# Performance work log

Measured on AMD Instinct MI355X. Metric: run time of the kernel, lower is better.

## Reference

```python
import jax, jax.numpy as jnp
import numpy as np

N = 50000          # nodes
E_RAND = 1_600_000 # random edges (avg degree 32)
IN = 8             # in_features
OUT = 8            # out_features
B = 16             # batch columns of x
T = 5              # edge types AFTER add_self_loops (type 1 = self loop, 2..5 = original)


def setup_inputs() -> dict:
    key = jax.random.key(0)
    k1, k2, k3, k4, k5, k6 = jax.random.split(key, 6)
    x = jax.random.normal(k1, (N * IN, B), jnp.float32)
    loops = jnp.arange(N, dtype=jnp.int32)
    # self loops prepended (type 1), random edges with types 2..T (original types shifted +1)
    src = jnp.concatenate([loops, jax.random.randint(k2, (E_RAND,), 0, N, jnp.int32)])
    dst = jnp.concatenate([loops, jax.random.randint(k3, (E_RAND,), 0, N, jnp.int32)])
    edge_types = jnp.concatenate([
        jnp.ones(N, jnp.int32),
        jax.random.randint(k4, (E_RAND,), 2, T + 1, jnp.int32),
    ])
    bound = 1.0 / np.sqrt(IN)
    # weight_vector reshaped: expand() maps ext_type = ((e-1)*OUT + i)*IN + j + 1
    W = jax.random.uniform(k5, (T, OUT, IN), jnp.float32, -bound, bound)
    # bias_vector reshaped: expand(OUT, 1) -> per (type, out-row) scalar
    Bv = jax.random.uniform(k6, (T, OUT), jnp.float32, -bound, bound)
    return dict(x=x, W=W, Bv=Bv, src=src, dst=dst, edge_types=edge_types)


def reference(x, W, Bv, src, dst, edge_types):
    T_, OUT_, IN_ = W.shape
    Nn = x.shape[0] // IN_
    xr = x.reshape(Nn, IN_, -1)                 # [N, in, B]
    Wg = W[edge_types - 1]                      # [E, out, in] per-edge weight block gather
    msg = jnp.einsum('eoi,eib->eob', Wg, xr[src])  # [E, out, B]
    y = jax.ops.segment_sum(msg, dst, num_segments=Nn)            # [N, out, B]
    yb = jax.ops.segment_sum(Bv[edge_types - 1], dst, num_segments=Nn)  # [N, out]
    y = y + yb[:, :, None]
    return y.reshape(Nn * OUT_, -1)             # [N*out, B]
```

## Files before the change

kernel.cpp:

```cpp
#include <hip/hip_runtime.h>
#include <hip/hip_fp16.h>

#define N_NODES 50000
#define E_RAND  1600000
#define IN_F    8
#define OUT_F   8
#define BATCH   16
#define T_TYPES 5

#define NB      782
#define CAP     2432
#define CHUNK   2048
#define BIN_BLOCKS  ((E_RAND + CHUNK - 1) / CHUNK)
#define CONV_BLOCKS 1563

#define OFF_BCUR   0
#define OFF_XH     4096
#define OFF_BINNED 12804096
#define WS_NEEDED  (OFF_BINNED + (size_t)NB * CAP * 4)

__global__ __launch_bounds__(512)
void zero_kernel(int* __restrict__ p, int n) {
    const int i = blockIdx.x * 512 + threadIdx.x;
    if (i < n) p[i] = 0;
}

__global__ __launch_bounds__(512)
void prep_kernel(const float* __restrict__ x, __half* __restrict__ xh,
                 const int* __restrict__ src, const int* __restrict__ dst,
                 const int* __restrict__ et,
                 int* __restrict__ bcur, int* __restrict__ binned) {
    if (blockIdx.x >= BIN_BLOCKS) {
        const int blk = blockIdx.x - BIN_BLOCKS;
        const int b = threadIdx.x & 15;
        const int n = blk * 32 + (threadIdx.x >> 4);
        if (n >= N_NODES) return;
        const float* xp = x + n * (IN_F * BATCH) + b;
        union { __half h[8]; uint4 u; } pk;
#pragma unroll
        for (int i = 0; i < IN_F; ++i) pk.h[i] = __float2half(xp[i * BATCH]);
        *(uint4*)(xh + (size_t)n * 128 + b * 8) = pk.u;
        return;
    }
    __shared__ int h[NB];
    __shared__ int rbase[NB];
    for (int i = threadIdx.x; i < NB; i += 512) h[i] = 0;
    __syncthreads();
    const int cbase = blockIdx.x * CHUNK;
#pragma unroll
    for (int k = 0; k < CHUNK / 512; ++k) {
        const int e = cbase + k * 512 + threadIdx.x;
        if (e < E_RAND) atomicAdd(&h[dst[N_NODES + e] >> 6], 1);
    }
    __syncthreads();
    for (int i = threadIdx.x; i < NB; i += 512) {
        const int c = h[i];
        rbase[i] = c ? atomicAdd(&bcur[i], c) : 0;
        h[i] = 0;
    }
    __syncthreads();
#pragma unroll
    for (int k = 0; k < CHUNK / 512; ++k) {
        const int e = cbase + k * 512 + threadIdx.x;
        if (e < E_RAND) {
            const int ee  = N_NODES + e;
            const int d   = dst[ee];
            const int bkt = d >> 6;
            const int payload = ((((d & 63) << 2) | (et[ee] - 2)) << 16) | src[ee];
            binned[bkt * CAP + rbase[bkt] + atomicAdd(&h[bkt], 1)] = payload;
        }
    }
}

__device__ __forceinline__ void unpack_add(uint4 v, float* xa) {
    const __half2* hp = (const __half2*)&v;
    float2 f;
    f = __half22float2(hp[0]); xa[0] += f.x; xa[1] += f.y;
    f = __half22float2(hp[1]); xa[2] += f.x; xa[3] += f.y;
    f = __half22float2(hp[2]); xa[4] += f.x; xa[5] += f.y;
    f = __half22float2(hp[3]); xa[6] += f.x; xa[7] += f.y;
}

__global__ __launch_bounds__(512)
void sortgather_kernel(const __half* __restrict__ xh,
                       const float* __restrict__ W,
                       const float* __restrict__ Bv,
                       const int* __restrict__ bcur,
                       const int* __restrict__ binned,
                       float* __restrict__ y) {
    __shared__ int   lraw[CAP];
    __shared__ int   lsort[CAP];
    __shared__ int   hist[256];
    __shared__ int   cur[256];
    __shared__ int   segoff[257];
    __shared__ float Wl[T_TYPES * OUT_F * IN_F];
    __shared__ float Bvl[T_TYPES * OUT_F];
    __shared__ int   wtot[4];

    const int bkt  = blockIdx.x;
    const int cnt  = bcur[bkt];
    const int base = bkt * CAP;
    const int t    = threadIdx.x;

    if (t < 320) Wl[t] = W[t];
    if (t >= 384 && t < 424) Bvl[t - 384] = Bv[t - 384];
    if (t < 256) hist[t] = 0;
    for (int i = t; i < cnt; i += 512) lraw[i] = binned[base + i];
    __syncthreads();

    for (int i = t; i < cnt; i += 512)
        atomicAdd(&hist[lraw[i] >> 16], 1);
    __syncthreads();

    if (t < 256) {
        const int lane = t & 63;
        int inc = hist[t];
#pragma unroll
        for (int d = 1; d < 64; d <<= 1) {
            const int u = __shfl_up(inc, d);
            if (lane >= d) inc += u;
        }
        cur[t] = inc;
        if (lane == 63) wtot[t >> 6] = inc;
    }
    __syncthreads();
    if (t < 256) {
        const int wv = t >> 6;
        int wbase = 0;
        for (int w = 0; w < wv; ++w) wbase += wtot[w];
        const int excl = wbase + cur[t] - hist[t];
        segoff[t] = excl;
        cur[t]    = excl;
        if (t == 255) segoff[256] = cnt;
    }
    __syncthreads();

    for (int i = t; i < cnt; i += 512) {
        const int p = lraw[i];
        lsort[atomicAdd(&cur[p >> 16], 1)] = p & 0xFFFF;
    }
    __syncthreads();

    const int gg   = t >> 4;
    const int b    = t & 15;
    const int boff = b * 8;

#pragma unroll
    for (int half = 0; half < 2; ++half) {
        const int ln = gg + half * 32;
        const int n  = bkt * 64 + ln;
        if (n >= N_NODES) continue;

        float xs[IN_F];
#pragma unroll
        for (int i = 0; i < IN_F; ++i) xs[i] = 0.f;
        unpack_add(*(const uint4*)(xh + (size_t)n * 128 + boff), xs);

        float out[OUT_F];
#pragma unroll
        for (int o = 0; o < OUT_F; ++o) {
            const float4 w0 = ((const float4*)(Wl + o * IN_F))[0];
            const float4 w1 = ((const float4*)(Wl + o * IN_F))[1];
            float a = Bvl[o];
            a = fmaf(w0.x, xs[0], a); a = fmaf(w0.y, xs[1], a);
            a = fmaf(w0.z, xs[2], a); a = fmaf(w0.w, xs[3], a);
            a = fmaf(w1.x, xs[4], a); a = fmaf(w1.y, xs[5], a);
            a = fmaf(w1.z, xs[6], a); a = fmaf(w1.w, xs[7], a);
            out[o] = a;
        }

        const int* sp = segoff + ln * 4;
#pragma unroll
        for (int t4 = 0; t4 < 4; ++t4) {
            const int s0 = sp[t4];
            const int s1 = sp[t4 + 1];
            const int c  = s1 - s0;
            if (c == 0) continue;

            float xa[IN_F];
#pragma unroll
            for (int i = 0; i < IN_F; ++i) xa[i] = 0.f;

            int e = s0;
            for (; e + 4 <= s1; e += 4) {
                const int i0 = lsort[e], i1 = lsort[e + 1];
                const int i2 = lsort[e + 2], i3 = lsort[e + 3];
                const uint4 r0 = *(const uint4*)(xh + (size_t)i0 * 128 + boff);
                const uint4 r1 = *(const uint4*)(xh + (size_t)i1 * 128 + boff);
                const uint4 r2 = *(const uint4*)(xh + (size_t)i2 * 128 + boff);
                const uint4 r3 = *(const uint4*)(xh + (size_t)i3 * 128 + boff);
                unpack_add(r0, xa); unpack_add(r1, xa);
                unpack_add(r2, xa); unpack_add(r3, xa);
            }
            for (; e < s1; ++e)
                unpack_add(*(const uint4*)(xh + (size_t)lsort[e] * 128 + boff), xa);

            const float* Wt = Wl + (t4 + 1) * (OUT_F * IN_F);
            const float* Bt = Bvl + (t4 + 1) * OUT_F;
            const float fc = (float)c;
#pragma unroll
            for (int o = 0; o < OUT_F; ++o) {
                const float4 w0 = ((const float4*)(Wt + o * IN_F))[0];
                const float4 w1 = ((const float4*)(Wt + o * IN_F))[1];
                float a = fmaf(fc, Bt[o], out[o]);
                a = fmaf(w0.x, xa[0], a); a = fmaf(w0.y, xa[1], a);
                a = fmaf(w0.z, xa[2], a); a = fmaf(w0.w, xa[3], a);
                a = fmaf(w1.x, xa[4], a); a = fmaf(w1.y, xa[5], a);
                a = fmaf(w1.z, xa[6], a); a = fmaf(w1.w, xa[7], a);
                out[o] = a;
            }
        }

        float* yp = y + (size_t)n * (OUT_F * BATCH) + b;
#pragma unroll
        for (int o = 0; o < OUT_F; ++o)
            yp[o * BATCH] = out[o];
    }
}

__global__ __launch_bounds__(256)
void selfinit_kernel(const float* __restrict__ x,
                     const float* __restrict__ W,
                     const float* __restrict__ Bv,
                     float* __restrict__ y) {
    const int b = threadIdx.x & (BATCH - 1);
    const int n = blockIdx.x * 16 + (threadIdx.x >> 4);
    if (n >= N_NODES) return;
    float xc[IN_F];
#pragma unroll
    for (int i = 0; i < IN_F; ++i) xc[i] = x[(n * IN_F + i) * BATCH + b];
#pragma unroll
    for (int o = 0; o < OUT_F; ++o) {
        float a = Bv[o];
#pragma unroll
        for (int i = 0; i < IN_F; ++i) a = fmaf(W[o * IN_F + i], xc[i], a);
        y[(n * OUT_F + o) * BATCH + b] = a;
    }
}

__global__ __launch_bounds__(256)
void direct_edge_kernel(const float* __restrict__ x,
                        const float* __restrict__ W,
                        const float* __restrict__ Bv,
                        const int* __restrict__ src,
                        const int* __restrict__ dst,
                        const int* __restrict__ et,
                        float* __restrict__ y) {
    const int tid = blockIdx.x * 256 + threadIdx.x;
    const int eg  = tid >> 4;
    const int b   = tid & (BATCH - 1);
    if (eg >= E_RAND) return;
    const int e  = N_NODES + eg;
    const int s  = src[e];
    const int d  = dst[e];
    const int ti = et[e] - 1;
    const float* __restrict__ Wt = W + ti * (OUT_F * IN_F);
    float xc[IN_F];
#pragma unroll
    for (int i = 0; i < IN_F; ++i) xc[i] = x[(s * IN_F + i) * BATCH + b];
    float* yp = y + (size_t)d * (OUT_F * BATCH) + b;
#pragma unroll
    for (int o = 0; o < OUT_F; ++o) {
        float a = Bv[ti * OUT_F + o];
#pragma unroll
        for (int i = 0; i < IN_F; ++i) a = fmaf(Wt[o * IN_F + i], xc[i], a);
        unsafeAtomicAdd(yp + o * BATCH, a);
    }
}

extern "C" void kernel_launch(void* const* d_in, const int* in_sizes, int n_in,
                              void* d_out, int out_size, void* d_ws, size_t ws_size,
                              hipStream_t stream) {
    const float* x   = (const float*)d_in[0];
    const float* W   = (const float*)d_in[1];
    const float* Bv  = (const float*)d_in[2];
    const int*   src = (const int*)d_in[3];
    const int*   dst = (const int*)d_in[4];
    const int*   et  = (const int*)d_in[5];
    float* y = (float*)d_out;

    char* ws = (char*)d_ws;
    int*    bcur   = (int*)(ws + OFF_BCUR);
    __half* xh     = (__half*)(ws + OFF_XH);
    int*    binned = (int*)(ws + OFF_BINNED);

    if (ws_size >= WS_NEEDED) {
        zero_kernel<<<2, 512, 0, stream>>>(bcur, NB);
        prep_kernel<<<BIN_BLOCKS + CONV_BLOCKS, 512, 0, stream>>>(x, xh, src, dst, et, bcur, binned);
        sortgather_kernel<<<NB, 512, 0, stream>>>(xh, W, Bv, bcur, binned, y);
    } else {
        selfinit_kernel<<<(N_NODES + 15) / 16, 256, 0, stream>>>(x, W, Bv, y);
        direct_edge_kernel<<<(E_RAND * 16 + 255) / 256, 256, 0, stream>>>(x, W, Bv, src, dst, et, y);
    }
}
```

Before: 195.0 us.

## Bin edges with partitioned global atomic counters instead of block histograms

Edge binning now does one global atomicAdd per edge into one of 8 partitioned counters per destination bucket. This replaces the two-pass shared-memory histogram and bulk reservation scheme. The gather kernel prefix-sums the 8 sub-bucket counts and compacts the sub-buckets into shared memory. The intent is to remove LDS passes and barriers, but it adds about 1.6M returning global atomics and larger workspace with fixed per-partition capacity.

```diff
diff --git a/kernel.cpp b/kernel.cpp
--- a/kernel.cpp
+++ b/kernel.cpp
@@ -8,16 +8,19 @@
 #define BATCH   16
 #define T_TYPES 5
 
-#define NB      782
-#define CAP     2432
-#define CHUNK   2048
-#define BIN_BLOCKS  ((E_RAND + CHUNK - 1) / CHUNK)
+#define NB       782
+#define NPART    8
+#define CAP_SUB  384
+#define CAPB     (NPART * CAP_SUB)
+#define LCAP     2560
+#define EPB      2048
+#define BIN_BLOCKS  ((E_RAND + EPB - 1) / EPB)
 #define CONV_BLOCKS 1563
 
 #define OFF_BCUR   0
-#define OFF_XH     4096
-#define OFF_BINNED 12804096
-#define WS_NEEDED  (OFF_BINNED + (size_t)NB * CAP * 4)
+#define OFF_XH     32768
+#define OFF_BINNED 12832768
+#define WS_NEEDED  (OFF_BINNED + (size_t)NB * CAPB * 4)
 
 __global__ __launch_bounds__(512)
 void zero_kernel(int* __restrict__ p, int n) {
@@ -30,46 +33,32 @@
                  const int* __restrict__ src, const int* __restrict__ dst,
                  const int* __restrict__ et,
                  int* __restrict__ bcur, int* __restrict__ binned) {
-    if (blockIdx.x >= BIN_BLOCKS) {
-        const int blk = blockIdx.x - BIN_BLOCKS;
-        const int b = threadIdx.x & 15;
-        const int n = blk * 32 + (threadIdx.x >> 4);
-        if (n >= N_NODES) return;
-        const float* xp = x + n * (IN_F * BATCH) + b;
-        union { __half h[8]; uint4 u; } pk;
-#pragma unroll
-        for (int i = 0; i < IN_F; ++i) pk.h[i] = __float2half(xp[i * BATCH]);
-        *(uint4*)(xh + (size_t)n * 128 + b * 8) = pk.u;
+    if (blockIdx.x < BIN_BLOCKS) {
+        const int part = blockIdx.x & (NPART - 1);
+        const int ebase = blockIdx.x * EPB + threadIdx.x;
+#pragma unroll
+        for (int k = 0; k < EPB / 512; ++k) {
+            const int e = ebase + k * 512;
+            if (e < E_RAND) {
+                const int ee  = N_NODES + e;
+                const int d   = dst[ee];
+                const int bkt = d >> 6;
+                const int payload = ((((d & 63) << 2) | (et[ee] - 2)) << 16) | src[ee];
+                const int pos = atomicAdd(&bcur[bkt * NPART + part], 1);
+                binned[bkt * CAPB + part * CAP_SUB + pos] = payload;
+            }
+        }
         return;
     }
-    __shared__ int h[NB];
-    __shared__ int rbase[NB];
-    for (int i = threadIdx.x; i < NB; i += 512) h[i] = 0;
-    __syncthreads();
-    const int cbase = blockIdx.x * CHUNK;
-#pragma unroll
-    for (int k = 0; k < CHUNK / 512; ++k) {
-        const int e = cbase + k * 512 + threadIdx.x;
-        if (e < E_RAND) atomicAdd(&h[dst[N_NODES + e] >> 6], 1);
-    }
-    __syncthreads();
-    for (int i = threadIdx.x; i < NB; i += 512) {
-        const int c = h[i];
-        rbase[i] = c ? atomicAdd(&bcur[i], c) : 0;
-        h[i] = 0;
-    }
-    __syncthreads();
-#pragma unroll
-    for (int k = 0; k < CHUNK / 512; ++k) {
-        const int e = cbase + k * 512 + threadIdx.x;
-        if (e < E_RAND) {
-            const int ee  = N_NODES + e;
-            const int d   = dst[ee];
-            const int bkt = d >> 6;
-            const int payload = ((((d & 63) << 2) | (et[ee] - 2)) << 16) | src[ee];
-            binned[bkt * CAP + rbase[bkt] + atomicAdd(&h[bkt], 1)] = payload;
-        }
-    }
+    const int blk = blockIdx.x - BIN_BLOCKS;
+    const int b = threadIdx.x & 15;
+    const int n = blk * 32 + (threadIdx.x >> 4);
+    if (n >= N_NODES) return;
+    const float* xp = x + n * (IN_F * BATCH) + b;
+    union { __half h[8]; uint4 u; } pk;
+#pragma unroll
+    for (int i = 0; i < IN_F; ++i) pk.h[i] = __float2half(xp[i * BATCH]);
+    *(uint4*)(xh + (size_t)n * 128 + b * 8) = pk.u;
 }
 
 __device__ __forceinline__ void unpack_add(uint4 v, float* xa) {
@@ -88,24 +77,38 @@
                        const int* __restrict__ bcur,
                        const int* __restrict__ binned,
                        float* __restrict__ y) {
-    __shared__ int   lraw[CAP];
-    __shared__ int   lsort[CAP];
+    __shared__ int   lraw[LCAP];
+    __shared__ int   lsort[LCAP];
     __shared__ int   hist[256];
     __shared__ int   cur[256];
     __shared__ int   segoff[257];
+    __shared__ int   ssub[NPART + 1];
     __shared__ float Wl[T_TYPES * OUT_F * IN_F];
     __shared__ float Bvl[T_TYPES * OUT_F];
     __shared__ int   wtot[4];
 
     const int bkt  = blockIdx.x;
-    const int cnt  = bcur[bkt];
-    const int base = bkt * CAP;
+    const int base = bkt * CAPB;
     const int t    = threadIdx.x;
 
     if (t < 320) Wl[t] = W[t];
     if (t >= 384 && t < 424) Bvl[t - 384] = Bv[t - 384];
     if (t < 256) hist[t] = 0;
-    for (int i = t; i < cnt; i += 512) lraw[i] = binned[base + i];
+    if (t < NPART) ssub[t + 1] = bcur[bkt * NPART + t];
+    __syncthreads();
+    if (t == 0) {
+        ssub[0] = 0;
+        for (int s = 0; s < NPART; ++s) ssub[s + 1] += ssub[s];
+    }
+    __syncthreads();
+    const int cnt = ssub[NPART];
+
+    for (int sub = 0; sub < NPART; ++sub) {
+        const int c0 = ssub[sub];
+        const int sc = ssub[sub + 1] - c0;
+        const int* bp = binned + base + sub * CAP_SUB;
+        for (int i = t; i < sc; i += 512) lraw[c0 + i] = bp[i];
+    }
     __syncthreads();
 
     for (int i = t; i < cnt; i += 512)
@@ -285,7 +288,7 @@
     int*    binned = (int*)(ws + OFF_BINNED);
 
     if (ws_size >= WS_NEEDED) {
-        zero_kernel<<<2, 512, 0, stream>>>(bcur, NB);
+        zero_kernel<<<(NB * NPART + 511) / 512, 512, 0, stream>>>(bcur, NB * NPART);
         prep_kernel<<<BIN_BLOCKS + CONV_BLOCKS, 512, 0, stream>>>(x, xh, src, dst, et, bcur, binned);
         sortgather_kernel<<<NB, 512, 0, stream>>>(xh, W, Bv, bcur, binned, y);
     } else {
```

Result: slower. 231.9 us (+18.9%).

## Fuse binning and gather into one cooperative kernel with two-level binning

Applied to the files above, without the earlier changes.

Replaces the three separate launches with a single cooperative kernel that uses grid-wide syncs between phases. Edge binning is split into two levels: 25 coarse superbuckets, then a second pass into the 782 fine buckets. This reduces global atomic contention and gives the scattered writes better locality. It also removes launch gaps, but adds three grid barriers, an extra pass over the edge payloads, and a limit on occupancy, since 1024 blocks of 512 threads must all be resident at once. A fallback path with four normal launches runs if the cooperative launch fails.

```diff
diff --git a/kernel.cpp b/kernel.cpp
--- a/kernel.cpp
+++ b/kernel.cpp
@@ -1,5 +1,8 @@
 #include <hip/hip_runtime.h>
 #include <hip/hip_fp16.h>
+#include <hip/hip_cooperative_groups.h>
+
+namespace cg = cooperative_groups;
 
 #define N_NODES 50000
 #define E_RAND  1600000
@@ -8,69 +11,36 @@
 #define BATCH   16
 #define T_TYPES 5
 
-#define NB      782
-#define CAP     2432
-#define CHUNK   2048
-#define BIN_BLOCKS  ((E_RAND + CHUNK - 1) / CHUNK)
-#define CONV_BLOCKS 1563
-
-#define OFF_BCUR   0
-#define OFF_XH     4096
-#define OFF_BINNED 12804096
-#define WS_NEEDED  (OFF_BINNED + (size_t)NB * CAP * 4)
-
-__global__ __launch_bounds__(512)
-void zero_kernel(int* __restrict__ p, int n) {
-    const int i = blockIdx.x * 512 + threadIdx.x;
-    if (i < n) p[i] = 0;
-}
-
-__global__ __launch_bounds__(512)
-void prep_kernel(const float* __restrict__ x, __half* __restrict__ xh,
-                 const int* __restrict__ src, const int* __restrict__ dst,
-                 const int* __restrict__ et,
-                 int* __restrict__ bcur, int* __restrict__ binned) {
-    if (blockIdx.x >= BIN_BLOCKS) {
-        const int blk = blockIdx.x - BIN_BLOCKS;
-        const int b = threadIdx.x & 15;
-        const int n = blk * 32 + (threadIdx.x >> 4);
-        if (n >= N_NODES) return;
-        const float* xp = x + n * (IN_F * BATCH) + b;
-        union { __half h[8]; uint4 u; } pk;
-#pragma unroll
-        for (int i = 0; i < IN_F; ++i) pk.h[i] = __float2half(xp[i * BATCH]);
-        *(uint4*)(xh + (size_t)n * 128 + b * 8) = pk.u;
-        return;
-    }
-    __shared__ int h[NB];
-    __shared__ int rbase[NB];
-    for (int i = threadIdx.x; i < NB; i += 512) h[i] = 0;
-    __syncthreads();
-    const int cbase = blockIdx.x * CHUNK;
-#pragma unroll
-    for (int k = 0; k < CHUNK / 512; ++k) {
-        const int e = cbase + k * 512 + threadIdx.x;
-        if (e < E_RAND) atomicAdd(&h[dst[N_NODES + e] >> 6], 1);
-    }
-    __syncthreads();
-    for (int i = threadIdx.x; i < NB; i += 512) {
-        const int c = h[i];
-        rbase[i] = c ? atomicAdd(&bcur[i], c) : 0;
-        h[i] = 0;
-    }
-    __syncthreads();
-#pragma unroll
-    for (int k = 0; k < CHUNK / 512; ++k) {
-        const int e = cbase + k * 512 + threadIdx.x;
-        if (e < E_RAND) {
-            const int ee  = N_NODES + e;
-            const int d   = dst[ee];
-            const int bkt = d >> 6;
-            const int payload = ((((d & 63) << 2) | (et[ee] - 2)) << 16) | src[ee];
-            binned[bkt * CAP + rbase[bkt] + atomicAdd(&h[bkt], 1)] = payload;
-        }
-    }
-}
+#define GRID    1024
+#define THREADS 512
+
+#define SB        25
+#define CAP_SB    67584
+#define NB        782
+#define CAPB      2432
+#define CA        1563
+#define NPB       49
+#define PB_PER_SB 25
+#define PB_CHUNK  2704
+#define PB_BLOCKS (SB * PB_PER_SB)
+
+#define OFF_BCUR1 0
+#define OFF_BCUR2 1024
+#define OFF_XH    8192
+#define OFF_BINA  12808192
+#define OFF_BIN2  19566592
+#define WS_NEEDED 27173888
+
+
+struct SmemP1 { int h[SB]; int rb[SB]; };
+struct SmemP2 { int sl[PB_CHUNK]; int h[32]; int rb[32]; };
+struct SmemP3 {
+    int   lraw[CAPB]; int lsort[CAPB];
+    int   hist[256]; int cur[256]; int segoff[257];
+    float Wl[T_TYPES * OUT_F * IN_F]; float Bvl[T_TYPES * OUT_F];
+    int   wtot[4];
+};
+union SmemU { SmemP1 p1; SmemP2 p2; SmemP3 p3; };
 
 __device__ __forceinline__ void unpack_add(uint4 v, float* xa) {
     const __half2* hp = (const __half2*)&v;
@@ -81,63 +51,119 @@
     f = __half22float2(hp[3]); xa[6] += f.x; xa[7] += f.y;
 }
 
-__global__ __launch_bounds__(512)
-void sortgather_kernel(const __half* __restrict__ xh,
-                       const float* __restrict__ W,
-                       const float* __restrict__ Bv,
-                       const int* __restrict__ bcur,
-                       const int* __restrict__ binned,
-                       float* __restrict__ y) {
-    __shared__ int   lraw[CAP];
-    __shared__ int   lsort[CAP];
-    __shared__ int   hist[256];
-    __shared__ int   cur[256];
-    __shared__ int   segoff[257];
-    __shared__ float Wl[T_TYPES * OUT_F * IN_F];
-    __shared__ float Bvl[T_TYPES * OUT_F];
-    __shared__ int   wtot[4];
-
-    const int bkt  = blockIdx.x;
-    const int cnt  = bcur[bkt];
-    const int base = bkt * CAP;
-    const int t    = threadIdx.x;
-
-    if (t < 320) Wl[t] = W[t];
-    if (t >= 384 && t < 424) Bvl[t - 384] = Bv[t - 384];
-    if (t < 256) hist[t] = 0;
-    for (int i = t; i < cnt; i += 512) lraw[i] = binned[base + i];
-    __syncthreads();
-
-    for (int i = t; i < cnt; i += 512)
-        atomicAdd(&hist[lraw[i] >> 16], 1);
+__device__ __forceinline__ void phase1(int blk, int t,
+    const float* __restrict__ x, __half* __restrict__ xh,
+    const int* __restrict__ src, const int* __restrict__ dst,
+    const int* __restrict__ et,
+    int* __restrict__ bcur1, int* __restrict__ binA, SmemP1& sm)
+{
+    const int e0 = blk * CA;
+    const int e1 = min(e0 + CA, E_RAND);
+    if (t < SB) sm.h[t] = 0;
+    __syncthreads();
+    for (int e = e0 + t; e < e1; e += THREADS)
+        atomicAdd(&sm.h[dst[N_NODES + e] >> 11], 1);
+    __syncthreads();
+    if (t < SB) {
+        const int c = sm.h[t];
+        sm.rb[t] = c ? atomicAdd(&bcur1[t], c) : 0;
+        sm.h[t] = 0;
+    }
+    __syncthreads();
+    for (int e = e0 + t; e < e1; e += THREADS) {
+        const int ee = N_NODES + e;
+        const int d  = dst[ee];
+        const int sb = d >> 11;
+        const int pa = ((d & 2047) << 18) | ((et[ee] - 2) << 16) | src[ee];
+        binA[sb * CAP_SB + sm.rb[sb] + atomicAdd(&sm.h[sb], 1)] = pa;
+    }
+    const int n0 = blk * NPB;
+    const int n1 = min(n0 + NPB, N_NODES);
+    const int b  = t & 15;
+    for (int n = n0 + (t >> 4); n < n1; n += THREADS / 16) {
+        const float* xp = x + n * (IN_F * BATCH) + b;
+        union { __half h[8]; uint4 u; } pk;
+#pragma unroll
+        for (int i = 0; i < IN_F; ++i) pk.h[i] = __float2half(xp[i * BATCH]);
+        *(uint4*)(xh + (size_t)n * 128 + b * 8) = pk.u;
+    }
+}
+
+__device__ __forceinline__ void phase2(int blk, int t,
+    const int* __restrict__ bcur1, const int* __restrict__ binA,
+    int* __restrict__ bcur2, int* __restrict__ bin2, SmemP2& sm)
+{
+    const int sb  = blk / PB_PER_SB;
+    const int j   = blk % PB_PER_SB;
+    const int cnt = bcur1[sb];
+    const int i0  = j * PB_CHUNK;
+    const int m   = min(i0 + PB_CHUNK, cnt) - i0;
+    if (m <= 0) return;
+    const int* bp = binA + sb * CAP_SB + i0;
+    for (int i = t; i < m; i += THREADS) sm.sl[i] = bp[i];
+    if (t < 32) sm.h[t] = 0;
+    __syncthreads();
+    for (int i = t; i < m; i += THREADS)
+        atomicAdd(&sm.h[sm.sl[i] >> 24], 1);
+    __syncthreads();
+    if (t < 32) {
+        const int c = sm.h[t];
+        sm.rb[t] = c ? atomicAdd(&bcur2[sb * 32 + t], c) : 0;
+        sm.h[t] = 0;
+    }
+    __syncthreads();
+    for (int i = t; i < m; i += THREADS) {
+        const int p  = sm.sl[i];
+        const int fb = p >> 24;
+        const int pb = (((((p >> 18) & 63) << 2) | ((p >> 16) & 3)) << 16) | (p & 0xFFFF);
+        bin2[(sb * 32 + fb) * CAPB + sm.rb[fb] + atomicAdd(&sm.h[fb], 1)] = pb;
+    }
+}
+
+__device__ __forceinline__ void phase3(int bkt, int t,
+    const __half* __restrict__ xh, const float* __restrict__ W,
+    const float* __restrict__ Bv, const int* __restrict__ bcur2,
+    const int* __restrict__ bin2, float* __restrict__ y, SmemP3& sm)
+{
+    const int cnt  = bcur2[bkt];
+    const int base = bkt * CAPB;
+
+    if (t < 320) sm.Wl[t] = W[t];
+    if (t >= 384 && t < 424) sm.Bvl[t - 384] = Bv[t - 384];
+    if (t < 256) sm.hist[t] = 0;
+    for (int i = t; i < cnt; i += THREADS) sm.lraw[i] = bin2[base + i];
+    __syncthreads();
+
+    for (int i = t; i < cnt; i += THREADS)
+        atomicAdd(&sm.hist[sm.lraw[i] >> 16], 1);
     __syncthreads();
 
     if (t < 256) {
         const int lane = t & 63;
-        int inc = hist[t];
+        int inc = sm.hist[t];
 #pragma unroll
         for (int d = 1; d < 64; d <<= 1) {
             const int u = __shfl_up(inc, d);
             if (lane >= d) inc += u;
         }
-        cur[t] = inc;
-        if (lane == 63) wtot[t >> 6] = inc;
+        sm.cur[t] = inc;
+        if (lane == 63) sm.wtot[t >> 6] = inc;
     }
     __syncthreads();
     if (t < 256) {
         const int wv = t >> 6;
         int wbase = 0;
-        for (int w = 0; w < wv; ++w) wbase += wtot[w];
-        const int excl = wbase + cur[t] - hist[t];
-        segoff[t] = excl;
-        cur[t]    = excl;
-        if (t == 255) segoff[256] = cnt;
-    }
-    __syncthreads();
-
-    for (int i = t; i < cnt; i += 512) {
-        const int p = lraw[i];
-        lsort[atomicAdd(&cur[p >> 16], 1)] = p & 0xFFFF;
+        for (int w = 0; w < wv; ++w) wbase += sm.wtot[w];
+        const int excl = wbase + sm.cur[t] - sm.hist[t];
+        sm.segoff[t] = excl;
+        sm.cur[t]    = excl;
+        if (t == 255) sm.segoff[256] = cnt;
+    }
+    __syncthreads();
+
+    for (int i = t; i < cnt; i += THREADS) {
+        const int p = sm.lraw[i];
+        sm.lsort[atomicAdd(&sm.cur[p >> 16], 1)] = p & 0xFFFF;
     }
     __syncthreads();
 
@@ -159,9 +185,9 @@
         float out[OUT_F];
 #pragma unroll
         for (int o = 0; o < OUT_F; ++o) {
-            const float4 w0 = ((const float4*)(Wl + o * IN_F))[0];
-            const float4 w1 = ((const float4*)(Wl + o * IN_F))[1];
-            float a = Bvl[o];
+            const float4 w0 = ((const float4*)(sm.Wl + o * IN_F))[0];
+            const float4 w1 = ((const float4*)(sm.Wl + o * IN_F))[1];
+            float a = sm.Bvl[o];
             a = fmaf(w0.x, xs[0], a); a = fmaf(w0.y, xs[1], a);
             a = fmaf(w0.z, xs[2], a); a = fmaf(w0.w, xs[3], a);
             a = fmaf(w1.x, xs[4], a); a = fmaf(w1.y, xs[5], a);
@@ -169,7 +195,7 @@
             out[o] = a;
         }
 
-        const int* sp = segoff + ln * 4;
+        const int* sp = sm.segoff + ln * 4;
 #pragma unroll
         for (int t4 = 0; t4 < 4; ++t4) {
             const int s0 = sp[t4];
@@ -183,8 +209,8 @@
 
             int e = s0;
             for (; e + 4 <= s1; e += 4) {
-                const int i0 = lsort[e], i1 = lsort[e + 1];
-                const int i2 = lsort[e + 2], i3 = lsort[e + 3];
+                const int i0 = sm.lsort[e],     i1 = sm.lsort[e + 1];
+                const int i2 = sm.lsort[e + 2], i3 = sm.lsort[e + 3];
                 const uint4 r0 = *(const uint4*)(xh + (size_t)i0 * 128 + boff);
                 const uint4 r1 = *(const uint4*)(xh + (size_t)i1 * 128 + boff);
                 const uint4 r2 = *(const uint4*)(xh + (size_t)i2 * 128 + boff);
@@ -193,10 +219,10 @@
                 unpack_add(r2, xa); unpack_add(r3, xa);
             }
             for (; e < s1; ++e)
-                unpack_add(*(const uint4*)(xh + (size_t)lsort[e] * 128 + boff), xa);
-
-            const float* Wt = Wl + (t4 + 1) * (OUT_F * IN_F);
-            const float* Bt = Bvl + (t4 + 1) * OUT_F;
+                unpack_add(*(const uint4*)(xh + (size_t)sm.lsort[e] * 128 + boff), xa);
+
+            const float* Wt = sm.Wl + (t4 + 1) * (OUT_F * IN_F);
+            const float* Bt = sm.Bvl + (t4 + 1) * OUT_F;
             const float fc = (float)c;
 #pragma unroll
             for (int o = 0; o < OUT_F; ++o) {
@@ -218,11 +244,54 @@
     }
 }
 
+__global__ __launch_bounds__(THREADS, 8)
+void fused_kernel(const float* __restrict__ x, const float* __restrict__ W,
+                  const float* __restrict__ Bv, const int* __restrict__ src,
+                  const int* __restrict__ dst, const int* __restrict__ et,
+                  int* bcur1, int* bcur2, __half* xh, int* binA, int* bin2,
+                  float* __restrict__ y)
+{
+    __shared__ SmemU sm;
+    cg::grid_group grid = cg::this_grid();
+    const int blk = blockIdx.x, t = threadIdx.x;
+
+    const int idx = blk * THREADS + t;
+    if (idx < SB) bcur1[idx] = 0;
+    if (idx < NB) bcur2[idx] = 0;
+    grid.sync();
+    phase1(blk, t, x, xh, src, dst, et, bcur1, binA, sm.p1);
+    grid.sync();
+    if (blk < PB_BLOCKS) phase2(blk, t, bcur1, binA, bcur2, bin2, sm.p2);
+    grid.sync();
+    if (blk < NB) phase3(blk, t, xh, W, Bv, bcur2, bin2, y, sm.p3);
+}
+
+__global__ __launch_bounds__(THREADS)
+void zero_k(int* bcur1, int* bcur2) {
+    const int idx = blockIdx.x * THREADS + threadIdx.x;
+    if (idx < SB) bcur1[idx] = 0;
+    if (idx < NB) bcur2[idx] = 0;
+}
+__global__ __launch_bounds__(THREADS)
+void prep_k(const float* x, __half* xh, const int* src, const int* dst,
+            const int* et, int* bcur1, int* binA) {
+    __shared__ SmemP1 s;
+    phase1(blockIdx.x, threadIdx.x, x, xh, src, dst, et, bcur1, binA, s);
+}
+__global__ __launch_bounds__(THREADS)
+void passb_k(const int* bcur1, const int* binA, int* bcur2, int* bin2) {
+    __shared__ SmemP2 s;
+    phase2(blockIdx.x, threadIdx.x, bcur1, binA, bcur2, bin2, s);
+}
+__global__ __launch_bounds__(THREADS)
+void sg_k(const __half* xh, const float* W, const float* Bv,
+          const int* bcur2, const int* bin2, float* y) {
+    __shared__ SmemP3 s;
+    phase3(blockIdx.x, threadIdx.x, xh, W, Bv, bcur2, bin2, y, s);
+}
+
 __global__ __launch_bounds__(256)
-void selfinit_kernel(const float* __restrict__ x,
-                     const float* __restrict__ W,
-                     const float* __restrict__ Bv,
-                     float* __restrict__ y) {
+void selfinit_kernel(const float* x, const float* W, const float* Bv, float* y) {
     const int b = threadIdx.x & (BATCH - 1);
     const int n = blockIdx.x * 16 + (threadIdx.x >> 4);
     if (n >= N_NODES) return;
@@ -237,15 +306,9 @@
         y[(n * OUT_F + o) * BATCH + b] = a;
     }
 }
-
 __global__ __launch_bounds__(256)
-void direct_edge_kernel(const float* __restrict__ x,
-                        const float* __restrict__ W,
-                        const float* __restrict__ Bv,
-                        const int* __restrict__ src,
-                        const int* __restrict__ dst,
-                        const int* __restrict__ et,
-                        float* __restrict__ y) {
+void direct_edge_kernel(const float* x, const float* W, const float* Bv,
+                        const int* src, const int* dst, const int* et, float* y) {
     const int tid = blockIdx.x * 256 + threadIdx.x;
     const int eg  = tid >> 4;
     const int b   = tid & (BATCH - 1);
@@ -254,7 +317,7 @@
     const int s  = src[e];
     const int d  = dst[e];
     const int ti = et[e] - 1;
-    const float* __restrict__ Wt = W + ti * (OUT_F * IN_F);
+    const float* Wt = W + ti * (OUT_F * IN_F);
     float xc[IN_F];
 #pragma unroll
     for (int i = 0; i < IN_F; ++i) xc[i] = x[(s * IN_F + i) * BATCH + b];
@@ -280,14 +343,25 @@
     float* y = (float*)d_out;
 
     char* ws = (char*)d_ws;
-    int*    bcur   = (int*)(ws + OFF_BCUR);
-    __half* xh     = (__half*)(ws + OFF_XH);
-    int*    binned = (int*)(ws + OFF_BINNED);
+    int*    bcur1 = (int*)(ws + OFF_BCUR1);
+    int*    bcur2 = (int*)(ws + OFF_BCUR2);
+    __half* xh    = (__half*)(ws + OFF_XH);
+    int*    binA  = (int*)(ws + OFF_BINA);
+    int*    bin2  = (int*)(ws + OFF_BIN2);
 
     if (ws_size >= WS_NEEDED) {
-        zero_kernel<<<2, 512, 0, stream>>>(bcur, NB);
-        prep_kernel<<<BIN_BLOCKS + CONV_BLOCKS, 512, 0, stream>>>(x, xh, src, dst, et, bcur, binned);
-        sortgather_kernel<<<NB, 512, 0, stream>>>(xh, W, Bv, bcur, binned, y);
+        void* kargs[] = {(void*)&x, (void*)&W, (void*)&Bv, (void*)&src,
+                         (void*)&dst, (void*)&et, (void*)&bcur1, (void*)&bcur2,
+                         (void*)&xh, (void*)&binA, (void*)&bin2, (void*)&y};
+        hipError_t rc = hipLaunchCooperativeKernel((const void*)fused_kernel,
+                                                   dim3(GRID), dim3(THREADS),
+                                                   kargs, 0, stream);
+        if (rc != hipSuccess) {
+            zero_k<<<2, THREADS, 0, stream>>>(bcur1, bcur2);
+            prep_k<<<GRID, THREADS, 0, stream>>>(x, xh, src, dst, et, bcur1, binA);
+            passb_k<<<PB_BLOCKS, THREADS, 0, stream>>>(bcur1, binA, bcur2, bin2);
+            sg_k<<<NB, THREADS, 0, stream>>>(xh, W, Bv, bcur2, bin2, y);
+        }
     } else {
         selfinit_kernel<<<(N_NODES + 15) / 16, 256, 0, stream>>>(x, W, Bv, y);
         direct_edge_kernel<<<(E_RAND * 16 + 255) / 256, 256, 0, stream>>>(x, W, Bv, src, dst, et, y);
```

Result: slower. 630.5 us (+223.3%).

## Split each node's edge gather across four lane groups with shuffle reduction

Applied to the files above, without the earlier changes.

The sort-gather stage now processes one node per group of 64 threads instead of one node per 16 threads. The four 16-lane subgroups each take every fourth edge of a type segment, combine their partial sums with cross-lane shuffles, and each compute two of the eight output rows. The goal is more parallel loads in flight per node and less per-thread serial latency, at the cost of shuffle work per type segment. The change also triples the binning chunk size, cutting the number of binning blocks, and replaces the zero kernel with a hipMemsetAsync.

```diff
diff --git a/kernel.cpp b/kernel.cpp
--- a/kernel.cpp
+++ b/kernel.cpp
@@ -10,7 +10,7 @@
 
 #define NB      782
 #define CAP     2432
-#define CHUNK   2048
+#define CHUNK   6144
 #define BIN_BLOCKS  ((E_RAND + CHUNK - 1) / CHUNK)
 #define CONV_BLOCKS 1563
 
@@ -18,12 +18,6 @@
 #define OFF_XH     4096
 #define OFF_BINNED 12804096
 #define WS_NEEDED  (OFF_BINNED + (size_t)NB * CAP * 4)
-
-__global__ __launch_bounds__(512)
-void zero_kernel(int* __restrict__ p, int n) {
-    const int i = blockIdx.x * 512 + threadIdx.x;
-    if (i < n) p[i] = 0;
-}
 
 __global__ __launch_bounds__(512)
 void prep_kernel(const float* __restrict__ x, __half* __restrict__ xh,
@@ -141,13 +135,15 @@
     }
     __syncthreads();
 
-    const int gg   = t >> 4;
-    const int b    = t & 15;
+    const int lane = t & 63;
+    const int w    = t >> 6;
+    const int g    = lane >> 4;
+    const int b    = lane & 15;
     const int boff = b * 8;
-
-#pragma unroll
-    for (int half = 0; half < 2; ++half) {
-        const int ln = gg + half * 32;
+    const int o0   = g * 2;
+
+    for (int k = 0; k < 8; ++k) {
+        const int ln = w * 8 + k;
         const int n  = bkt * 64 + ln;
         if (n >= N_NODES) continue;
 
@@ -156,9 +152,10 @@
         for (int i = 0; i < IN_F; ++i) xs[i] = 0.f;
         unpack_add(*(const uint4*)(xh + (size_t)n * 128 + boff), xs);
 
-        float out[OUT_F];
-#pragma unroll
-        for (int o = 0; o < OUT_F; ++o) {
+        float out[2];
+#pragma unroll
+        for (int c = 0; c < 2; ++c) {
+            const int o = o0 + c;
             const float4 w0 = ((const float4*)(Wl + o * IN_F))[0];
             const float4 w1 = ((const float4*)(Wl + o * IN_F))[1];
             float a = Bvl[o];
@@ -166,7 +163,7 @@
             a = fmaf(w0.z, xs[2], a); a = fmaf(w0.w, xs[3], a);
             a = fmaf(w1.x, xs[4], a); a = fmaf(w1.y, xs[5], a);
             a = fmaf(w1.z, xs[6], a); a = fmaf(w1.w, xs[7], a);
-            out[o] = a;
+            out[c] = a;
         }
 
         const int* sp = segoff + ln * 4;
@@ -181,40 +178,43 @@
 #pragma unroll
             for (int i = 0; i < IN_F; ++i) xa[i] = 0.f;
 
-            int e = s0;
-            for (; e + 4 <= s1; e += 4) {
-                const int i0 = lsort[e], i1 = lsort[e + 1];
-                const int i2 = lsort[e + 2], i3 = lsort[e + 3];
+            int e = s0 + g;
+            for (; e + 4 < s1; e += 8) {
+                const int i0 = lsort[e];
+                const int i1 = lsort[e + 4];
                 const uint4 r0 = *(const uint4*)(xh + (size_t)i0 * 128 + boff);
                 const uint4 r1 = *(const uint4*)(xh + (size_t)i1 * 128 + boff);
-                const uint4 r2 = *(const uint4*)(xh + (size_t)i2 * 128 + boff);
-                const uint4 r3 = *(const uint4*)(xh + (size_t)i3 * 128 + boff);
                 unpack_add(r0, xa); unpack_add(r1, xa);
-                unpack_add(r2, xa); unpack_add(r3, xa);
             }
-            for (; e < s1; ++e)
+            if (e < s1)
                 unpack_add(*(const uint4*)(xh + (size_t)lsort[e] * 128 + boff), xa);
+
+#pragma unroll
+            for (int i = 0; i < IN_F; ++i) {
+                xa[i] += __shfl_xor(xa[i], 16);
+                xa[i] += __shfl_xor(xa[i], 32);
+            }
 
             const float* Wt = Wl + (t4 + 1) * (OUT_F * IN_F);
             const float* Bt = Bvl + (t4 + 1) * OUT_F;
             const float fc = (float)c;
 #pragma unroll
-            for (int o = 0; o < OUT_F; ++o) {
+            for (int cc = 0; cc < 2; ++cc) {
+                const int o = o0 + cc;
                 const float4 w0 = ((const float4*)(Wt + o * IN_F))[0];
                 const float4 w1 = ((const float4*)(Wt + o * IN_F))[1];
-                float a = fmaf(fc, Bt[o], out[o]);
+                float a = fmaf(fc, Bt[o], out[cc]);
                 a = fmaf(w0.x, xa[0], a); a = fmaf(w0.y, xa[1], a);
                 a = fmaf(w0.z, xa[2], a); a = fmaf(w0.w, xa[3], a);
                 a = fmaf(w1.x, xa[4], a); a = fmaf(w1.y, xa[5], a);
                 a = fmaf(w1.z, xa[6], a); a = fmaf(w1.w, xa[7], a);
-                out[o] = a;
+                out[cc] = a;
             }
         }
 
         float* yp = y + (size_t)n * (OUT_F * BATCH) + b;
-#pragma unroll
-        for (int o = 0; o < OUT_F; ++o)
-            yp[o * BATCH] = out[o];
+        yp[(o0    ) * BATCH] = out[0];
+        yp[(o0 + 1) * BATCH] = out[1];
     }
 }
 
@@ -285,7 +285,7 @@
     int*    binned = (int*)(ws + OFF_BINNED);
 
     if (ws_size >= WS_NEEDED) {
-        zero_kernel<<<2, 512, 0, stream>>>(bcur, NB);
+        hipMemsetAsync(bcur, 0, NB * sizeof(int), stream);
         prep_kernel<<<BIN_BLOCKS + CONV_BLOCKS, 512, 0, stream>>>(x, xh, src, dst, et, bcur, binned);
         sortgather_kernel<<<NB, 512, 0, stream>>>(xh, W, Bv, bcur, binned, y);
     } else {
```

New measurement: 196.0 us. No clear change (+0.5%).
